# Kernel tuning notes

Measured on AMD Instinct MI355X. Metric: run time of the kernel, lower is better.

The kernel has to match this reference:

```python
import jax, jax.numpy as jnp
import numpy as np

B, L, D = 2, 2048, 1024
H, DK, DV = 16, 64, 64
EPS = 1e-6

def setup_inputs() -> dict:
    key = jax.random.key(0)
    ks = jax.random.split(key, 10)
    s = 0.02
    q = jax.random.normal(ks[0], (B, L, D), jnp.float32)
    k = jax.random.normal(ks[1], (B, L, D), jnp.float32)
    v = jax.random.normal(ks[2], (B, L, D), jnp.float32)
    mask = jax.random.uniform(ks[3], (B, L, L)) < 0.95  # bool [B, Lq, Lk]
    w_q = jax.random.normal(ks[4], (D, H * DK), jnp.float32) * s
    w_k = jax.random.normal(ks[5], (D, H * DK), jnp.float32) * s
    w_v = jax.random.normal(ks[6], (D, H * DV), jnp.float32) * s
    w_o = jax.random.normal(ks[7], (H * DV, D), jnp.float32) * s
    ln_g = jnp.ones((D,), jnp.float32)
    ln_b = jnp.zeros((D,), jnp.float32)
    return {"q": q, "k": k, "v": v, "mask": mask,
            "w_q": w_q, "w_k": w_k, "w_v": w_v, "w_o": w_o,
            "ln_g": ln_g, "ln_b": ln_b}

def reference(q, k, v, mask, w_q, w_k, w_v, w_o, ln_g, ln_b):
    residual = q
    # QKV projections -> [B, H, L, d]
    qh = (q @ w_q).reshape(B, L, H, DK).transpose(0, 2, 1, 3)
    kh = (k @ w_k).reshape(B, L, H, DK).transpose(0, 2, 1, 3)
    vh = (v @ w_v).reshape(B, L, H, DV).transpose(0, 2, 1, 3)
    temp = jnp.asarray(DK, jnp.float32) ** 0.5
    # scores [B, H, Lq, Lk]
    scores = jnp.einsum('bhqd,bhkd->bhqk', qh / temp, kh)
    scores = jnp.where(mask[:, None, :, :], scores, -1e9)
    attn = jax.nn.softmax(scores, axis=-1)  # dropout = identity (eval)
    out = jnp.einsum('bhqk,bhkd->bhqd', attn, vh)
    out = out.transpose(0, 2, 1, 3).reshape(B, L, H * DV)
    out = out @ w_o + residual
    # LayerNorm, eps=1e-6
    mu = jnp.mean(out, axis=-1, keepdims=True)
    var = jnp.var(out, axis=-1, keepdims=True)
    out = (out - mu) * jax.lax.rsqrt(var + EPS) * ln_g + ln_b
    return out, attn
```

## Files before the change

kernel.cpp:

```cpp
#include <hip/hip_runtime.h>

#define B_ 2
#define L_ 2048
#define D_ 1024
#define H_ 16
#define DK_ 64

typedef __bf16 bf16x8 __attribute__((ext_vector_type(8)));
typedef short s16x8 __attribute__((ext_vector_type(8)));
typedef float f32x4 __attribute__((ext_vector_type(4)));

__device__ inline f32x4 mfma_bf16(s16x8 a, s16x8 b, f32x4 c) {
    return __builtin_amdgcn_mfma_f32_16x16x32_bf16(
        __builtin_bit_cast(bf16x8, a), __builtin_bit_cast(bf16x8, b), c, 0, 0, 0);
}

__device__ inline unsigned short f2bf(float f) {
    unsigned int x = __builtin_bit_cast(unsigned int, f);
    unsigned int r = (x + 0x7fffu + ((x >> 16) & 1u)) >> 16;
    return (unsigned short)r;
}

__device__ inline s16x8 cvt8(const float* __restrict__ p) {
    s16x8 r;
#pragma unroll
    for (int j = 0; j < 8; ++j) r[j] = (short)f2bf(p[j]);
    return r;
}

__global__ __launch_bounds__(256) void transpose_w(const float* __restrict__ src,
                                                   unsigned short* __restrict__ dst) {
    int idx = blockIdx.x * 256 + threadIdx.x;
    int k = idx >> 10, n = idx & 1023;
    dst[n * 1024 + k] = f2bf(src[idx]);
}

template <int MODE>
__global__ __launch_bounds__(256) void gemm_f32a(const float* __restrict__ X,
                                                 const unsigned short* __restrict__ WT,
                                                 unsigned short* __restrict__ out) {
    int wave = threadIdx.x >> 6;
    int lane = threadIdx.x & 63;
    int l15 = lane & 15, quad = lane >> 4;
    int mrow = blockIdx.x * 64 + wave * 16 + l15;
    int ntbase = blockIdx.y * 64;

    const float* aptr = X + mrow * 1024 + quad * 8;
    f32x4 acc[4];
#pragma unroll
    for (int d = 0; d < 4; ++d) acc[d] = (f32x4){0.f, 0.f, 0.f, 0.f};

    for (int k0 = 0; k0 < 1024; k0 += 32) {
        s16x8 a = cvt8(aptr + k0);
#pragma unroll
        for (int d = 0; d < 4; ++d) {
            const unsigned short* bptr = WT + (ntbase + d * 16 + l15) * 1024 + k0 + quad * 8;
            acc[d] = mfma_bf16(a, *(const s16x8*)bptr, acc[d]);
        }
    }

    int mbase = blockIdx.x * 64 + wave * 16 + quad * 4;
#pragma unroll
    for (int d = 0; d < 4; ++d) {
        int ncol = ntbase + d * 16 + l15;
#pragma unroll
        for (int r = 0; r < 4; ++r) {
            int m = mbase + r;
            float vv = acc[d][r];
            int b = m >> 11, l = m & 2047, h = ncol >> 6, dd = ncol & 63;
            if (MODE == 0) {
                out[(((b * H_ + h) * L_) + l) * DK_ + dd] = f2bf(vv);
            } else {
                out[(((b * H_ + h) * DK_) + dd) * L_ + l] = f2bf(vv);
            }
        }
    }
}

__global__ __launch_bounds__(256) void gemm_bf16a(const unsigned short* __restrict__ X,
                                                  const unsigned short* __restrict__ WT,
                                                  float* __restrict__ out) {
    int wave = threadIdx.x >> 6;
    int lane = threadIdx.x & 63;
    int l15 = lane & 15, quad = lane >> 4;
    int mrow = blockIdx.x * 64 + wave * 16 + l15;
    int ntbase = blockIdx.y * 64;

    const unsigned short* aptr = X + mrow * 1024 + quad * 8;
    f32x4 acc[4];
#pragma unroll
    for (int d = 0; d < 4; ++d) acc[d] = (f32x4){0.f, 0.f, 0.f, 0.f};

    for (int k0 = 0; k0 < 1024; k0 += 32) {
        s16x8 a = *(const s16x8*)(aptr + k0);
#pragma unroll
        for (int d = 0; d < 4; ++d) {
            const unsigned short* bptr = WT + (ntbase + d * 16 + l15) * 1024 + k0 + quad * 8;
            acc[d] = mfma_bf16(a, *(const s16x8*)bptr, acc[d]);
        }
    }

    int mbase = blockIdx.x * 64 + wave * 16 + quad * 4;
#pragma unroll
    for (int d = 0; d < 4; ++d) {
        int ncol = ntbase + d * 16 + l15;
#pragma unroll
        for (int r = 0; r < 4; ++r)
            out[(mbase + r) * 1024 + ncol] = acc[d][r];
    }
}

__global__ __launch_bounds__(256) void attn_kernel(const unsigned short* __restrict__ qh,
                                                   const unsigned short* __restrict__ kh,
                                                   const unsigned short* __restrict__ vt,
                                                   const int* __restrict__ mask,
                                                   float* __restrict__ attn,
                                                   unsigned short* __restrict__ ctx) {
    __shared__ unsigned short pbuf[4][16][32];
    int wave = threadIdx.x >> 6, lane = threadIdx.x & 63;
    int l15 = lane & 15, quad = lane >> 4;
    int bh = blockIdx.x >> 5;
    int qt = blockIdx.x & 31;
    int b = bh >> 4;
    int q0 = qt * 64 + wave * 16;

    const unsigned short* Q = qh + (bh * L_ + q0 + l15) * DK_ + quad * 8;
    const unsigned short* K = kh + (size_t)bh * L_ * DK_;
    s16x8 a0 = *(const s16x8*)(Q);
    s16x8 a1 = *(const s16x8*)(Q + 32);

    const int* mrow[4];
#pragma unroll
    for (int r = 0; r < 4; ++r)
        mrow[r] = mask + (size_t)(b * L_ + q0 + quad * 4 + r) * L_;

    float m_l[4], l_l[4];
#pragma unroll
    for (int r = 0; r < 4; ++r) { m_l[r] = -1e30f; l_l[r] = 0.f; }

    for (int kt = 0; kt < 128; ++kt) {
        int col = kt * 16 + l15;
        const unsigned short* Kp = K + col * DK_ + quad * 8;
        f32x4 acc = (f32x4){0.f, 0.f, 0.f, 0.f};
        acc = mfma_bf16(a0, *(const s16x8*)Kp, acc);
        acc = mfma_bf16(a1, *(const s16x8*)(Kp + 32), acc);
#pragma unroll
        for (int r = 0; r < 4; ++r) {
            float sv = mrow[r][col] ? acc[r] * 0.125f : -1e9f;
            float mo = m_l[r];
            float mn = fmaxf(mo, sv);
            l_l[r] = l_l[r] * __expf(mo - mn) + __expf(sv - mn);
            m_l[r] = mn;
        }
    }
    float Mf[4], inv_l[4];
#pragma unroll
    for (int r = 0; r < 4; ++r) {
        float mM = m_l[r];
        mM = fmaxf(mM, __shfl_xor(mM, 1));
        mM = fmaxf(mM, __shfl_xor(mM, 2));
        mM = fmaxf(mM, __shfl_xor(mM, 4));
        mM = fmaxf(mM, __shfl_xor(mM, 8));
        float la = l_l[r] * __expf(m_l[r] - mM);
        la += __shfl_xor(la, 1);
        la += __shfl_xor(la, 2);
        la += __shfl_xor(la, 4);
        la += __shfl_xor(la, 8);
        Mf[r] = mM;
        inv_l[r] = 1.0f / la;
    }

    float* arow[4];
#pragma unroll
    for (int r = 0; r < 4; ++r)
        arow[r] = attn + ((size_t)bh * L_ + q0 + quad * 4 + r) * L_;

    f32x4 oacc[4];
#pragma unroll
    for (int d = 0; d < 4; ++d) oacc[d] = (f32x4){0.f, 0.f, 0.f, 0.f};

    for (int c = 0; c < 64; ++c) {
        int n0 = c * 32;
#pragma unroll
        for (int t = 0; t < 2; ++t) {
            int col = n0 + t * 16 + l15;
            const unsigned short* Kp = K + col * DK_ + quad * 8;
            f32x4 acc = (f32x4){0.f, 0.f, 0.f, 0.f};
            acc = mfma_bf16(a0, *(const s16x8*)Kp, acc);
            acc = mfma_bf16(a1, *(const s16x8*)(Kp + 32), acc);
#pragma unroll
            for (int r = 0; r < 4; ++r) {
                float sv = mrow[r][col] ? acc[r] * 0.125f : -1e9f;
                float p = __expf(sv - Mf[r]) * inv_l[r];
                arow[r][col] = p;
                pbuf[wave][quad * 4 + r][t * 16 + l15] = f2bf(p);
            }
        }
        __syncthreads();
        s16x8 pa = *(const s16x8*)&pbuf[wave][l15][quad * 8];
#pragma unroll
        for (int d = 0; d < 4; ++d) {
            const unsigned short* Vp = vt + ((size_t)bh * DK_ + d * 16 + l15) * L_ + n0 + quad * 8;
            oacc[d] = mfma_bf16(pa, *(const s16x8*)Vp, oacc[d]);
        }
        __syncthreads();
    }

    int h = bh & 15;
#pragma unroll
    for (int d = 0; d < 4; ++d) {
#pragma unroll
        for (int r = 0; r < 4; ++r) {
            int l = q0 + quad * 4 + r;
            ctx[((size_t)(b * L_ + l)) * 1024 + h * 64 + d * 16 + l15] = f2bf(oacc[d][r]);
        }
    }
}

__global__ __launch_bounds__(256) void ln_kernel(const float* __restrict__ pre,
                                                 const float* __restrict__ resid,
                                                 const float* __restrict__ g,
                                                 const float* __restrict__ beta,
                                                 float* __restrict__ out) {
    int row = blockIdx.x;
    int tid = threadIdx.x;
    const float* pr = pre + (size_t)row * 1024;
    const float* rr = resid + (size_t)row * 1024;
    float x[4], s = 0.f, sq = 0.f;
#pragma unroll
    for (int i = 0; i < 4; ++i) {
        int idx = tid + i * 256;
        x[i] = pr[idx] + rr[idx];
        s += x[i];
        sq += x[i] * x[i];
    }
    s += __shfl_xor(s, 1);  sq += __shfl_xor(sq, 1);
    s += __shfl_xor(s, 2);  sq += __shfl_xor(sq, 2);
    s += __shfl_xor(s, 4);  sq += __shfl_xor(sq, 4);
    s += __shfl_xor(s, 8);  sq += __shfl_xor(sq, 8);
    s += __shfl_xor(s, 16); sq += __shfl_xor(sq, 16);
    s += __shfl_xor(s, 32); sq += __shfl_xor(sq, 32);
    __shared__ float ssum[4], ssq[4];
    if ((tid & 63) == 0) { ssum[tid >> 6] = s; ssq[tid >> 6] = sq; }
    __syncthreads();
    s = ssum[0] + ssum[1] + ssum[2] + ssum[3];
    sq = ssq[0] + ssq[1] + ssq[2] + ssq[3];
    float mean = s * (1.0f / 1024.0f);
    float var = sq * (1.0f / 1024.0f) - mean * mean;
    float rstd = rsqrtf(var + 1e-6f);
#pragma unroll
    for (int i = 0; i < 4; ++i) {
        int idx = tid + i * 256;
        out[(size_t)row * 1024 + idx] = (x[i] - mean) * rstd * g[idx] + beta[idx];
    }
}

extern "C" void kernel_launch(void* const* d_in, const int* in_sizes, int n_in,
                              void* d_out, int out_size, void* d_ws, size_t ws_size,
                              hipStream_t stream) {
    const float* q   = (const float*)d_in[0];
    const float* k   = (const float*)d_in[1];
    const float* v   = (const float*)d_in[2];
    const int*   msk = (const int*)d_in[3];
    const float* w_q = (const float*)d_in[4];
    const float* w_k = (const float*)d_in[5];
    const float* w_v = (const float*)d_in[6];
    const float* w_o = (const float*)d_in[7];
    const float* lng = (const float*)d_in[8];
    const float* lnb = (const float*)d_in[9];

    char* ws = (char*)d_ws;
    unsigned short* wqT = (unsigned short*)(ws + 0 * (1u << 21));
    unsigned short* wkT = (unsigned short*)(ws + 1 * (1u << 21));
    unsigned short* wvT = (unsigned short*)(ws + 2 * (1u << 21));
    unsigned short* woT = (unsigned short*)(ws + 3 * (1u << 21));
    unsigned short* qh  = (unsigned short*)(ws + (8u << 20));
    unsigned short* kh  = (unsigned short*)(ws + (16u << 20));
    unsigned short* vt  = (unsigned short*)(ws + (24u << 20));
    unsigned short* ctx = (unsigned short*)(ws + (32u << 20));
    float*          pre = (float*)(ws + (8u << 20));

    float* outp = (float*)d_out;
    float* attn = outp + (size_t)B_ * L_ * D_;

    transpose_w<<<4096, 256, 0, stream>>>(w_q, wqT);
    transpose_w<<<4096, 256, 0, stream>>>(w_k, wkT);
    transpose_w<<<4096, 256, 0, stream>>>(w_v, wvT);
    transpose_w<<<4096, 256, 0, stream>>>(w_o, woT);

    dim3 g1(64, 16);
    gemm_f32a<0><<<g1, 256, 0, stream>>>(q, wqT, qh);
    gemm_f32a<0><<<g1, 256, 0, stream>>>(k, wkT, kh);
    gemm_f32a<1><<<g1, 256, 0, stream>>>(v, wvT, vt);

    attn_kernel<<<1024, 256, 0, stream>>>(qh, kh, vt, msk, attn, ctx);

    gemm_bf16a<<<g1, 256, 0, stream>>>(ctx, woT, pre);

    ln_kernel<<<4096, 256, 0, stream>>>(pre, q, lng, lnb, outp);
}
```

Baseline: 1.300 ms.

## Tile GEMMs through LDS, fuse QKV launches, drop softmax max pass

Replaces the per-wave global-memory GEMMs with a 128x128 LDS-tiled GEMM that uses swizzled shared memory and register prefetch of the next K slice, and merges the three QKV projections into one launch. In attention, the online max tracking is dropped so the softmax is computed as exp(s)/sum without max subtraction, the P buffer gets padding, and the block-wide barriers around it are removed. Skipping the max is numerically unsafe for large scores, though here scores are small. Removing the barriers relies on each wave writing and reading only its own pbuf slice.

```diff
diff --git a/kernel.cpp b/kernel.cpp
--- a/kernel.cpp
+++ b/kernel.cpp
@@ -21,11 +21,16 @@
     return (unsigned short)r;
 }
 
-__device__ inline s16x8 cvt8(const float* __restrict__ p) {
+__device__ __forceinline__ s16x8 ldA8(const float* __restrict__ p) {
+    f32x4 lo = *(const f32x4*)p;
+    f32x4 hi = *(const f32x4*)(p + 4);
     s16x8 r;
 #pragma unroll
-    for (int j = 0; j < 8; ++j) r[j] = (short)f2bf(p[j]);
+    for (int j = 0; j < 4; ++j) { r[j] = (short)f2bf(lo[j]); r[j + 4] = (short)f2bf(hi[j]); }
     return r;
+}
+__device__ __forceinline__ s16x8 ldA8(const unsigned short* __restrict__ p) {
+    return *(const s16x8*)p;
 }
 
 __global__ __launch_bounds__(256) void transpose_w(const float* __restrict__ src,
@@ -35,79 +40,115 @@
     dst[n * 1024 + k] = f2bf(src[idx]);
 }
 
-template <int MODE>
-__global__ __launch_bounds__(256) void gemm_f32a(const float* __restrict__ X,
-                                                 const unsigned short* __restrict__ WT,
-                                                 unsigned short* __restrict__ out) {
-    int wave = threadIdx.x >> 6;
-    int lane = threadIdx.x & 63;
+template <typename AT>
+__device__ __forceinline__ void gemm_core(const AT* __restrict__ A,
+                                          const unsigned short* __restrict__ BT,
+                                          unsigned short* __restrict__ outb,
+                                          float* __restrict__ outf, int mode) {
+    __shared__ unsigned short As[128 * 32];
+    __shared__ unsigned short Bs[128 * 32];
+    int tid = threadIdx.x;
+    int wave = tid >> 6, lane = tid & 63;
     int l15 = lane & 15, quad = lane >> 4;
-    int mrow = blockIdx.x * 64 + wave * 16 + l15;
-    int ntbase = blockIdx.y * 64;
-
-    const float* aptr = X + mrow * 1024 + quad * 8;
-    f32x4 acc[4];
-#pragma unroll
-    for (int d = 0; d < 4; ++d) acc[d] = (f32x4){0.f, 0.f, 0.f, 0.f};
+    int wm = wave >> 1, wn = wave & 1;
+    int m0 = blockIdx.x * 128;
+    int n0 = blockIdx.y * 128;
+
+    int f0 = wave * 1024 + lane * 8;
+    int f1 = f0 + 512;
+    int r0 = f0 >> 5, c0 = f0 & 31;
+    int r1 = f1 >> 5, c1 = f1 & 31;
+    int sw0 = r0 * 32 + ((((c0 >> 3) ^ ((r0 >> 1) & 3))) << 3);
+    int sw1 = r1 * 32 + ((((c1 >> 3) ^ ((r1 >> 1) & 3))) << 3);
+
+    const AT* ga0 = A + (size_t)(m0 + r0) * 1024 + c0;
+    const AT* ga1 = A + (size_t)(m0 + r1) * 1024 + c1;
+    const unsigned short* gb0 = BT + (size_t)(n0 + r0) * 1024 + c0;
+    const unsigned short* gb1 = BT + (size_t)(n0 + r1) * 1024 + c1;
+
+    f32x4 acc[4][4];
+#pragma unroll
+    for (int i = 0; i < 4; ++i)
+#pragma unroll
+        for (int j = 0; j < 4; ++j) acc[i][j] = (f32x4){0.f, 0.f, 0.f, 0.f};
+
+    int rsw = ((l15 >> 1) & 3) ^ quad;
+
+    s16x8 ra0 = ldA8(ga0), ra1 = ldA8(ga1);
+    s16x8 rb0 = ldA8(gb0), rb1 = ldA8(gb1);
 
     for (int k0 = 0; k0 < 1024; k0 += 32) {
-        s16x8 a = cvt8(aptr + k0);
-#pragma unroll
-        for (int d = 0; d < 4; ++d) {
-            const unsigned short* bptr = WT + (ntbase + d * 16 + l15) * 1024 + k0 + quad * 8;
-            acc[d] = mfma_bf16(a, *(const s16x8*)bptr, acc[d]);
-        }
-    }
-
-    int mbase = blockIdx.x * 64 + wave * 16 + quad * 4;
-#pragma unroll
-    for (int d = 0; d < 4; ++d) {
-        int ncol = ntbase + d * 16 + l15;
-#pragma unroll
-        for (int r = 0; r < 4; ++r) {
-            int m = mbase + r;
-            float vv = acc[d][r];
-            int b = m >> 11, l = m & 2047, h = ncol >> 6, dd = ncol & 63;
-            if (MODE == 0) {
-                out[(((b * H_ + h) * L_) + l) * DK_ + dd] = f2bf(vv);
-            } else {
-                out[(((b * H_ + h) * DK_) + dd) * L_ + l] = f2bf(vv);
+        __syncthreads();
+        *(s16x8*)&As[sw0] = ra0;
+        *(s16x8*)&As[sw1] = ra1;
+        *(s16x8*)&Bs[sw0] = rb0;
+        *(s16x8*)&Bs[sw1] = rb1;
+        __syncthreads();
+
+        if (k0 + 32 < 1024) {
+            ra0 = ldA8(ga0 + k0 + 32);
+            ra1 = ldA8(ga1 + k0 + 32);
+            rb0 = ldA8(gb0 + k0 + 32);
+            rb1 = ldA8(gb1 + k0 + 32);
+        }
+
+        s16x8 af[4], bfr[4];
+#pragma unroll
+        for (int t = 0; t < 4; ++t) {
+            af[t]  = *(const s16x8*)&As[(wm * 64 + t * 16 + l15) * 32 + rsw * 8];
+            bfr[t] = *(const s16x8*)&Bs[(wn * 64 + t * 16 + l15) * 32 + rsw * 8];
+        }
+#pragma unroll
+        for (int i = 0; i < 4; ++i)
+#pragma unroll
+            for (int j = 0; j < 4; ++j)
+                acc[i][j] = mfma_bf16(af[i], bfr[j], acc[i][j]);
+    }
+
+#pragma unroll
+    for (int i = 0; i < 4; ++i) {
+        int mb = m0 + wm * 64 + i * 16 + quad * 4;
+#pragma unroll
+        for (int j = 0; j < 4; ++j) {
+            int n = n0 + wn * 64 + j * 16 + l15;
+#pragma unroll
+            for (int r = 0; r < 4; ++r) {
+                int m = mb + r;
+                float vv = acc[i][j][r];
+                if (mode == 2) {
+                    outf[(size_t)m * 1024 + n] = vv;
+                } else {
+                    int b = m >> 11, l = m & 2047, h = n >> 6, dd = n & 63;
+                    if (mode == 0)
+                        outb[(((size_t)(b * H_ + h) * L_) + l) * DK_ + dd] = f2bf(vv);
+                    else
+                        outb[(((size_t)(b * H_ + h) * DK_) + dd) * L_ + l] = f2bf(vv);
+                }
             }
         }
     }
 }
 
-__global__ __launch_bounds__(256) void gemm_bf16a(const unsigned short* __restrict__ X,
-                                                  const unsigned short* __restrict__ WT,
-                                                  float* __restrict__ out) {
-    int wave = threadIdx.x >> 6;
-    int lane = threadIdx.x & 63;
-    int l15 = lane & 15, quad = lane >> 4;
-    int mrow = blockIdx.x * 64 + wave * 16 + l15;
-    int ntbase = blockIdx.y * 64;
-
-    const unsigned short* aptr = X + mrow * 1024 + quad * 8;
-    f32x4 acc[4];
-#pragma unroll
-    for (int d = 0; d < 4; ++d) acc[d] = (f32x4){0.f, 0.f, 0.f, 0.f};
-
-    for (int k0 = 0; k0 < 1024; k0 += 32) {
-        s16x8 a = *(const s16x8*)(aptr + k0);
-#pragma unroll
-        for (int d = 0; d < 4; ++d) {
-            const unsigned short* bptr = WT + (ntbase + d * 16 + l15) * 1024 + k0 + quad * 8;
-            acc[d] = mfma_bf16(a, *(const s16x8*)bptr, acc[d]);
-        }
-    }
-
-    int mbase = blockIdx.x * 64 + wave * 16 + quad * 4;
-#pragma unroll
-    for (int d = 0; d < 4; ++d) {
-        int ncol = ntbase + d * 16 + l15;
-#pragma unroll
-        for (int r = 0; r < 4; ++r)
-            out[(mbase + r) * 1024 + ncol] = acc[d][r];
-    }
+__global__ __launch_bounds__(256) void qkv_gemm(const float* __restrict__ q,
+                                                const float* __restrict__ k,
+                                                const float* __restrict__ v,
+                                                const unsigned short* __restrict__ wqT,
+                                                const unsigned short* __restrict__ wkT,
+                                                const unsigned short* __restrict__ wvT,
+                                                unsigned short* __restrict__ qh,
+                                                unsigned short* __restrict__ kh,
+                                                unsigned short* __restrict__ vt) {
+    int z = blockIdx.z;
+    const float* A           = (z == 0) ? q : (z == 1) ? k : v;
+    const unsigned short* BT = (z == 0) ? wqT : (z == 1) ? wkT : wvT;
+    unsigned short* o        = (z == 0) ? qh : (z == 1) ? kh : vt;
+    gemm_core<float>(A, BT, o, nullptr, (z == 2) ? 1 : 0);
+}
+
+__global__ __launch_bounds__(256) void oproj_gemm(const unsigned short* __restrict__ ctx,
+                                                  const unsigned short* __restrict__ woT,
+                                                  float* __restrict__ pre) {
+    gemm_core<unsigned short>(ctx, woT, nullptr, pre, 2);
 }
 
 __global__ __launch_bounds__(256) void attn_kernel(const unsigned short* __restrict__ qh,
@@ -116,7 +157,7 @@
                                                    const int* __restrict__ mask,
                                                    float* __restrict__ attn,
                                                    unsigned short* __restrict__ ctx) {
-    __shared__ unsigned short pbuf[4][16][32];
+    __shared__ unsigned short pbuf[4][16][40];
     int wave = threadIdx.x >> 6, lane = threadIdx.x & 63;
     int l15 = lane & 15, quad = lane >> 4;
     int bh = blockIdx.x >> 5;
@@ -134,10 +175,7 @@
     for (int r = 0; r < 4; ++r)
         mrow[r] = mask + (size_t)(b * L_ + q0 + quad * 4 + r) * L_;
 
-    float m_l[4], l_l[4];
-#pragma unroll
-    for (int r = 0; r < 4; ++r) { m_l[r] = -1e30f; l_l[r] = 0.f; }
-
+    float l_l[4] = {0.f, 0.f, 0.f, 0.f};
     for (int kt = 0; kt < 128; ++kt) {
         int col = kt * 16 + l15;
         const unsigned short* Kp = K + col * DK_ + quad * 8;
@@ -147,26 +185,17 @@
 #pragma unroll
         for (int r = 0; r < 4; ++r) {
             float sv = mrow[r][col] ? acc[r] * 0.125f : -1e9f;
-            float mo = m_l[r];
-            float mn = fmaxf(mo, sv);
-            l_l[r] = l_l[r] * __expf(mo - mn) + __expf(sv - mn);
-            m_l[r] = mn;
-        }
-    }
-    float Mf[4], inv_l[4];
+            l_l[r] += __expf(sv);
+        }
+    }
+    float inv_l[4];
 #pragma unroll
     for (int r = 0; r < 4; ++r) {
-        float mM = m_l[r];
-        mM = fmaxf(mM, __shfl_xor(mM, 1));
-        mM = fmaxf(mM, __shfl_xor(mM, 2));
-        mM = fmaxf(mM, __shfl_xor(mM, 4));
-        mM = fmaxf(mM, __shfl_xor(mM, 8));
-        float la = l_l[r] * __expf(m_l[r] - mM);
+        float la = l_l[r];
         la += __shfl_xor(la, 1);
         la += __shfl_xor(la, 2);
         la += __shfl_xor(la, 4);
         la += __shfl_xor(la, 8);
-        Mf[r] = mM;
         inv_l[r] = 1.0f / la;
     }
 
@@ -191,19 +220,17 @@
 #pragma unroll
             for (int r = 0; r < 4; ++r) {
                 float sv = mrow[r][col] ? acc[r] * 0.125f : -1e9f;
-                float p = __expf(sv - Mf[r]) * inv_l[r];
+                float p = __expf(sv) * inv_l[r];
                 arow[r][col] = p;
                 pbuf[wave][quad * 4 + r][t * 16 + l15] = f2bf(p);
             }
         }
-        __syncthreads();
         s16x8 pa = *(const s16x8*)&pbuf[wave][l15][quad * 8];
 #pragma unroll
         for (int d = 0; d < 4; ++d) {
             const unsigned short* Vp = vt + ((size_t)bh * DK_ + d * 16 + l15) * L_ + n0 + quad * 8;
             oacc[d] = mfma_bf16(pa, *(const s16x8*)Vp, oacc[d]);
         }
-        __syncthreads();
     }
 
     int h = bh & 15;
@@ -280,22 +307,21 @@
     unsigned short* ctx = (unsigned short*)(ws + (32u << 20));
     float*          pre = (float*)(ws + (8u << 20));
 
-    float* outp = (float*)d_out;
-    float* attn = outp + (size_t)B_ * L_ * D_;
+    float* outp  = (float*)d_out;
+    float* attnf = outp + (size_t)B_ * L_ * D_;
 
     transpose_w<<<4096, 256, 0, stream>>>(w_q, wqT);
     transpose_w<<<4096, 256, 0, stream>>>(w_k, wkT);
     transpose_w<<<4096, 256, 0, stream>>>(w_v, wvT);
     transpose_w<<<4096, 256, 0, stream>>>(w_o, woT);
 
-    dim3 g1(64, 16);
-    gemm_f32a<0><<<g1, 256, 0, stream>>>(q, wqT, qh);
-    gemm_f32a<0><<<g1, 256, 0, stream>>>(k, wkT, kh);
-    gemm_f32a<1><<<g1, 256, 0, stream>>>(v, wvT, vt);
-
-    attn_kernel<<<1024, 256, 0, stream>>>(qh, kh, vt, msk, attn, ctx);
-
-    gemm_bf16a<<<g1, 256, 0, stream>>>(ctx, woT, pre);
+    dim3 gq(32, 8, 3);
+    qkv_gemm<<<gq, 256, 0, stream>>>(q, k, v, wqT, wkT, wvT, qh, kh, vt);
+
+    attn_kernel<<<1024, 256, 0, stream>>>(qh, kh, vt, msk, attnf, ctx);
+
+    dim3 go(32, 8);
+    oproj_gemm<<<go, 256, 0, stream>>>(ctx, woT, pre);
 
     ln_kernel<<<4096, 256, 0, stream>>>(pre, q, lng, lnb, outp);
 }
```

After: 1.073 ms. -17.4%, faster.
